# Optimization experiments

Measured on AMD Instinct MI355X. Metric: run time of the kernel, lower is better.

The kernel has to match this reference:

```python
import jax, jax.numpy as jnp
import numpy as np

N = 320      # points per coordinate axis
RANK = 64    # CP rank = features[-1]
H = 128      # hidden width
DIMS = 3     # input_dim


def setup_inputs() -> dict:
    key = jax.random.key(0)
    ks = jax.random.split(key, 6)
    s0 = (6.0 / (1 + H)) ** 0.5   # xavier-uniform-ish scale for 1->H
    s1 = (6.0 / (H + H)) ** 0.5
    s2 = (6.0 / (H + RANK)) ** 0.5
    return {
        "xs": jax.random.normal(ks[0], (DIMS, N, 1), dtype=jnp.float32),
        "W0": jax.random.uniform(ks[1], (DIMS, 1, H), jnp.float32, -s0, s0),
        "b0": jnp.zeros((DIMS, H), jnp.float32),
        "W1": jax.random.uniform(ks[2], (DIMS, H, H), jnp.float32, -s1, s1),
        "b1": jnp.zeros((DIMS, H), jnp.float32),
        "W2": jax.random.uniform(ks[3], (DIMS, H, H), jnp.float32, -s1, s1),
        "b2": jnp.zeros((DIMS, H), jnp.float32),
        "W3": jax.random.uniform(ks[4], (DIMS, H, RANK), jnp.float32, -s2, s2),
        "b3": jnp.zeros((DIMS, RANK), jnp.float32),
    }


def reference(xs, W0, b0, W1, b1, W2, b2, W3, b3):
    # Per-coordinate MLP (identical to independent Dense stacks in the flax loop),
    # vmapped over the DIMS leading axis of stacked params.
    def mlp(x, w0, bb0, w1, bb1, w2, bb2, w3, bb3):
        h = jnp.tanh(x @ w0 + bb0)          # (N, H)
        h = jnp.tanh(h @ w1 + bb1)          # (N, H)
        h = jnp.tanh(h @ w2 + bb2)          # (N, H)
        return h @ w3 + bb3                 # (N, R)

    outs = jax.vmap(mlp)(xs, W0, b0, W1, b1, W2, b2, W3, b3)  # (DIMS, N, R)
    f = jnp.transpose(outs, (0, 2, 1))                         # (DIMS, R, N)
    # CP reconstruction: 'ra,rb,rc->abc' over shared rank r
    return jnp.einsum('ra,rb,rc->abc', f[0], f[1], f[2])
```

## Files before the change

kernel.cpp:

```cpp
#include <hip/hip_runtime.h>
#include <math.h>

#define DIMS 3
#define NPTS 320
#define HID  128
#define RANK 64
#define CH   160
#define LROW 128

typedef __attribute__((ext_vector_type(8)))  short bf16x8;
typedef __attribute__((ext_vector_type(16))) float f32x16;

static __device__ __forceinline__ unsigned short f2bf_rn(float x) {
    union { float f; unsigned int u; } v; v.f = x;
    unsigned int r = v.u + 0x7fffu + ((v.u >> 16) & 1u);
    return (unsigned short)(r >> 16);
}
static __device__ __forceinline__ float bf2f(unsigned short h) {
    union { unsigned int u; float f; } v; v.u = ((unsigned int)h) << 16;
    return v.f;
}

__global__ __launch_bounds__(512)
void mlp_kernel(const float* __restrict__ xs,
                const float* __restrict__ W0, const float* __restrict__ b0,
                const float* __restrict__ W1, const float* __restrict__ b1,
                const float* __restrict__ W2, const float* __restrict__ b2,
                const float* __restrict__ W3, const float* __restrict__ b3,
                float* __restrict__ f01t,
                unsigned short* __restrict__ f2hi) {
    const int blk = blockIdx.x;
    const int d = blk / NPTS, n = blk % NPTS;
    const int j  = threadIdx.x & (HID - 1);
    const int kq = threadIdx.x >> 7;
    const int k0 = kq * 32;

    __shared__ float ha[HID];
    __shared__ float hb[HID];
    __shared__ float part[4][HID];

    const float x = xs[d * NPTS + n];

    if (kq == 0) {
        ha[j] = tanhf(fmaf(x, W0[d * HID + j], b0[d * HID + j]));
    }
    __syncthreads();

    {
        float acc = 0.0f;
        const float* w = W1 + d * HID * HID + j;
        #pragma unroll 16
        for (int k = 0; k < 32; ++k) acc = fmaf(ha[k0 + k], w[(k0 + k) * HID], acc);
        part[kq][j] = acc;
    }
    __syncthreads();
    if (kq == 0) {
        float s = ((part[0][j] + part[1][j]) + (part[2][j] + part[3][j]))
                  + b1[d * HID + j];
        hb[j] = tanhf(s);
    }
    __syncthreads();

    {
        float acc = 0.0f;
        const float* w = W2 + d * HID * HID + j;
        #pragma unroll 16
        for (int k = 0; k < 32; ++k) acc = fmaf(hb[k0 + k], w[(k0 + k) * HID], acc);
        part[kq][j] = acc;
    }
    __syncthreads();
    if (kq == 0) {
        float s = ((part[0][j] + part[1][j]) + (part[2][j] + part[3][j]))
                  + b2[d * HID + j];
        ha[j] = tanhf(s);
    }
    __syncthreads();

    if (j < RANK) {
        float acc = 0.0f;
        const float* w = W3 + d * HID * RANK + j;
        #pragma unroll 16
        for (int k = 0; k < 32; ++k) acc = fmaf(ha[k0 + k], w[(k0 + k) * RANK], acc);
        part[kq][j] = acc;
    }
    __syncthreads();
    if (kq == 0 && j < RANK) {
        float s = ((part[0][j] + part[1][j]) + (part[2][j] + part[3][j]))
                  + b3[d * RANK + j];
        if (d == 0) {
            f01t[n * RANK + j] = s;
        } else if (d == 1) {
            f01t[(NPTS + n) * RANK + j] = s;
        } else {
            f2hi[n * RANK + j] = f2bf_rn(s);
        }
    }
}

__global__ __launch_bounds__(128, 2)
void cp_mfma_kernel(const float* __restrict__ f01t,
                    const unsigned short* __restrict__ f2hi,
                    float* __restrict__ out) {
    const int tx = threadIdx.x;
    const int w  = tx >> 6;
    const int l  = tx & 63;
    const int lc = l & 31;
    const int hw = l >> 5;

    const int c0 = (blockIdx.x & 1) * CH;

    __shared__ char sB[CH * LROW];

    #pragma unroll
    for (int i = 0; i < 10; ++i) {
        int idx = tx + i * 128;
        int row = idx >> 3;
        int g   = (idx & 7) << 4;
        *(float4*)(&sB[row * LROW + (g ^ ((row & 7) << 4))]) =
            ((const float4*)f2hi)[c0 * 8 + idx];
    }
    __syncthreads();

    for (int t = blockIdx.x >> 1; t < NPTS * 5; t += 512) {
        const int a   = t / 5;
        const int b0w = (t - a * 5) * 64 + w * 32;
        const float* f0p = f01t + (size_t)a * RANK + hw * 8;
        const float* f1p = f01t + (size_t)(NPTS + b0w + lc) * RANK + hw * 8;

        bf16x8 ahi[4], alo[4];
        #pragma unroll
        for (int ks = 0; ks < 4; ++ks) {
            const int k0 = ks * 16;
            float4 f0a = *(const float4*)(f0p + k0);
            float4 f0b = *(const float4*)(f0p + k0 + 4);
            float4 f1a = *(const float4*)(f1p + k0);
            float4 f1b = *(const float4*)(f1p + k0 + 4);

            float g[8];
            g[0] = f1a.x * f0a.x; g[1] = f1a.y * f0a.y;
            g[2] = f1a.z * f0a.z; g[3] = f1a.w * f0a.w;
            g[4] = f1b.x * f0b.x; g[5] = f1b.y * f0b.y;
            g[6] = f1b.z * f0b.z; g[7] = f1b.w * f0b.w;

            #pragma unroll
            for (int j = 0; j < 8; ++j) {
                unsigned short hi = f2bf_rn(g[j]);
                ahi[ks][j] = (short)hi;
                alo[ks][j] = (short)f2bf_rn(g[j] - bf2f(hi));
            }
        }

        #pragma unroll
        for (int ct = 0; ct < 5; ++ct) {
            const char* rowp = &sB[(ct * 32 + lc) * LROW];
            const int swz = ((ct * 32 + lc) & 7) << 4;

            f32x16 acc;
            #pragma unroll
            for (int jj = 0; jj < 16; ++jj) acc[jj] = 0.0f;

            #pragma unroll
            for (int ks = 0; ks < 4; ++ks) {
                const int base = ks * 32 + (hw << 4);
                bf16x8 b = *(const bf16x8*)(rowp + (base ^ swz));
                acc = __builtin_amdgcn_mfma_f32_32x32x16_bf16(ahi[ks], b, acc, 0, 0, 0);
                acc = __builtin_amdgcn_mfma_f32_32x32x16_bf16(alo[ks], b, acc, 0, 0, 0);
            }

            float* obase = out + ((size_t)a * NPTS + b0w) * NPTS + c0 + ct * 32 + lc;
            #pragma unroll
            for (int q = 0; q < 16; ++q) {
                int row = (q & 3) + 8 * (q >> 2) + 4 * hw;
                obase[(size_t)row * NPTS] = acc[q];
            }
        }
    }
}

extern "C" void kernel_launch(void* const* d_in, const int* in_sizes, int n_in,
                              void* d_out, int out_size, void* d_ws, size_t ws_size,
                              hipStream_t stream) {
    const float* xs = (const float*)d_in[0];
    const float* W0 = (const float*)d_in[1];
    const float* b0 = (const float*)d_in[2];
    const float* W1 = (const float*)d_in[3];
    const float* b1 = (const float*)d_in[4];
    const float* W2 = (const float*)d_in[5];
    const float* b2 = (const float*)d_in[6];
    const float* W3 = (const float*)d_in[7];
    const float* b3 = (const float*)d_in[8];

    float* f01t = (float*)d_ws;
    unsigned short* f2hi = (unsigned short*)((char*)d_ws + 2 * NPTS * RANK * 4);
    float* out = (float*)d_out;

    mlp_kernel<<<dim3(DIMS * NPTS), dim3(512), 0, stream>>>(
        xs, W0, b0, W1, b1, W2, b2, W3, b3, f01t, f2hi);

    cp_mfma_kernel<<<dim3(1024), dim3(128), 0, stream>>>(f01t, f2hi, out);
}
```

Before: 37.90 us.

## Stage CP output tiles in LDS and write full rows with coalesced float4 stores

Each block now holds the entire bf16 f2 factor (all 320 c columns) in LDS and processes a 32×320 output tile per iteration. Results go into a 40KB LDS staging buffer and are then written to global memory as contiguous float4 rows, replacing the scattered per-lane scalar stores. The grid is halved to 512 blocks. In exchange, LDS use rises to about 80KB per block, which limits occupancy, and two block-wide barriers are added to every tile iteration.

```diff
diff --git a/kernel.cpp b/kernel.cpp
--- a/kernel.cpp
+++ b/kernel.cpp
@@ -5,8 +5,8 @@
 #define NPTS 320
 #define HID  128
 #define RANK 64
-#define CH   160
 #define LROW 128
+#define NTILE (NPTS * 10)
 
 typedef __attribute__((ext_vector_type(8)))  short bf16x8;
 typedef __attribute__((ext_vector_type(16))) float f32x16;
@@ -107,25 +107,24 @@
     const int lc = l & 31;
     const int hw = l >> 5;
 
-    const int c0 = (blockIdx.x & 1) * CH;
-
-    __shared__ char sB[CH * LROW];
+    __shared__ char  sB[NPTS * LROW];
+    __shared__ float stage[32 * NPTS];
 
     #pragma unroll
-    for (int i = 0; i < 10; ++i) {
+    for (int i = 0; i < 20; ++i) {
         int idx = tx + i * 128;
         int row = idx >> 3;
         int g   = (idx & 7) << 4;
         *(float4*)(&sB[row * LROW + (g ^ ((row & 7) << 4))]) =
-            ((const float4*)f2hi)[c0 * 8 + idx];
-    }
-    __syncthreads();
-
-    for (int t = blockIdx.x >> 1; t < NPTS * 5; t += 512) {
-        const int a   = t / 5;
-        const int b0w = (t - a * 5) * 64 + w * 32;
+            ((const float4*)f2hi)[idx];
+    }
+    __syncthreads();
+
+    for (int t = blockIdx.x; t < NTILE; t += 512) {
+        const int a  = t / 10;
+        const int b0 = (t - a * 10) * 32;
         const float* f0p = f01t + (size_t)a * RANK + hw * 8;
-        const float* f1p = f01t + (size_t)(NPTS + b0w + lc) * RANK + hw * 8;
+        const float* f1p = f01t + (size_t)(NPTS + b0 + lc) * RANK + hw * 8;
 
         bf16x8 ahi[4], alo[4];
         #pragma unroll
@@ -152,8 +151,9 @@
 
         #pragma unroll
         for (int ct = 0; ct < 5; ++ct) {
-            const char* rowp = &sB[(ct * 32 + lc) * LROW];
-            const int swz = ((ct * 32 + lc) & 7) << 4;
+            const int crow = w * 160 + ct * 32 + lc;
+            const char* rowp = &sB[crow * LROW];
+            const int swz = (crow & 7) << 4;
 
             f32x16 acc;
             #pragma unroll
@@ -167,13 +167,24 @@
                 acc = __builtin_amdgcn_mfma_f32_32x32x16_bf16(alo[ks], b, acc, 0, 0, 0);
             }
 
-            float* obase = out + ((size_t)a * NPTS + b0w) * NPTS + c0 + ct * 32 + lc;
             #pragma unroll
             for (int q = 0; q < 16; ++q) {
                 int row = (q & 3) + 8 * (q >> 2) + 4 * hw;
-                obase[(size_t)row * NPTS] = acc[q];
-            }
-        }
+                stage[row * NPTS + crow] = acc[q];
+            }
+        }
+        __syncthreads();
+
+        {
+            float* obase = out + ((size_t)a * NPTS + b0) * NPTS;
+            const float4* src = (const float4*)stage;
+            float4* dst = (float4*)obase;
+            #pragma unroll
+            for (int p = 0; p < 20; ++p) {
+                dst[tx + p * 128] = src[tx + p * 128];
+            }
+        }
+        __syncthreads();
     }
 }
 
@@ -197,5 +208,5 @@
     mlp_kernel<<<dim3(DIMS * NPTS), dim3(512), 0, stream>>>(
         xs, W0, b0, W1, b1, W2, b2, W3, b3, f01t, f2hi);
 
-    cp_mfma_kernel<<<dim3(1024), dim3(128), 0, stream>>>(f01t, f2hi, out);
-}
+    cp_mfma_kernel<<<dim3(512), dim3(128), 0, stream>>>(f01t, f2hi, out);
+}
```

Measured after the change: 40.61 us. 1.07x slower.
